# Performance work log

Measured on AMD Instinct MI355X. Metric: run time of the kernel, lower is better.

## Reference

```python
import jax, jax.numpy as jnp
import numpy as np

EMBED = 2048
HEADS = 16
HEAD_DIM = EMBED // HEADS
BATCH = 4
SEQ = 2048


def setup_inputs() -> dict:
    key = jax.random.key(0)
    ks = jax.random.split(key, 9)
    s = 1.0 / np.sqrt(EMBED)
    return {
        "x": jax.random.normal(ks[0], (BATCH, SEQ, EMBED), jnp.float32),
        "q_w": jax.random.normal(ks[1], (EMBED, EMBED), jnp.float32) * s,
        "q_b": jax.random.normal(ks[2], (EMBED,), jnp.float32) * 0.01,
        "k_w": jax.random.normal(ks[3], (EMBED, EMBED), jnp.float32) * s,
        "k_b": jax.random.normal(ks[4], (EMBED,), jnp.float32) * 0.01,
        "v_w": jax.random.normal(ks[5], (EMBED, EMBED), jnp.float32) * s,
        "v_b": jax.random.normal(ks[6], (EMBED,), jnp.float32) * 0.01,
        "o_w": jax.random.normal(ks[7], (EMBED, EMBED), jnp.float32) * s,
        "o_b": jax.random.normal(ks[8], (EMBED,), jnp.float32) * 0.01,
    }


def _split_heads(t):
    B, S, _ = t.shape
    return t.reshape(B, S, HEADS, HEAD_DIM).transpose(0, 2, 1, 3)  # [B,H,S,D]


def reference(x, q_w, q_b, k_w, k_b, v_w, v_b, o_w, o_b):
    B, S, E = x.shape
    q = _split_heads(x @ q_w.T + q_b)
    k = _split_heads(x @ k_w.T + k_b)
    v = _split_heads(x @ v_w.T + v_b)
    scores = jnp.einsum("bhsd,bhtd->bhst", q, k) / np.sqrt(HEAD_DIM).astype(np.float32)
    # ALiBi bias: slopes_i = -2^(-(8-i)); bias = -|s-t| * slope  (faithful to source)
    slopes = jnp.asarray([-2.0 ** (-(8 - i)) for i in range(HEADS)], jnp.float32)
    pos = jnp.arange(S)
    rel = -jnp.abs(pos[None, :] - pos[:, None]).astype(jnp.float32)  # [S,S]
    scores = scores + rel[None, None] * slopes[None, :, None, None]
    attn = jax.nn.softmax(scores, axis=-1)
    out = jnp.einsum("bhst,bhtd->bhsd", attn, v)
    out = out.transpose(0, 2, 1, 3).reshape(B, S, E)
    return out @ o_w.T + o_b
```

## Files before the change

### kernel.cpp

```cpp
#include <hip/hip_runtime.h>

#define EMBED 2048
#define HEADS 16
#define HDIM  128
#define BATCH 4
#define SEQ   2048
#define MROWS (BATCH*SEQ)

typedef __attribute__((ext_vector_type(8))) _Float16 h8;
typedef __attribute__((ext_vector_type(4))) _Float16 h4;
typedef __attribute__((ext_vector_type(4))) float     f32x4;

__device__ inline f32x4 mfma16(h8 a, h8 b, f32x4 c){
  return __builtin_amdgcn_mfma_f32_16x16x32_f16(a, b, c, 0, 0, 0);
}

__device__ inline void gl_lds16(const void* g, void* l){
  __builtin_amdgcn_global_load_lds(
      (__attribute__((address_space(1))) unsigned*)g,
      (__attribute__((address_space(3))) unsigned*)l, 16, 0, 0);
}

__global__ __launch_bounds__(256) void f2h_kernel(const float* __restrict__ src,
                                                  _Float16* __restrict__ dst, int n){
  int stride = gridDim.x * blockDim.x * 8;
  for (int i = (blockIdx.x*blockDim.x + threadIdx.x)*8; i < n; i += stride){
    f32x4 a = *(const f32x4*)(src + i);
    f32x4 b = *(const f32x4*)(src + i + 4);
    h8 o;
    o[0]=(_Float16)a[0]; o[1]=(_Float16)a[1]; o[2]=(_Float16)a[2]; o[3]=(_Float16)a[3];
    o[4]=(_Float16)b[0]; o[5]=(_Float16)b[1]; o[6]=(_Float16)b[2]; o[7]=(_Float16)b[3];
    *(h8*)(dst + i) = o;
  }
}

template<int MODE>
__global__ __launch_bounds__(256) void gemm_bt(const _Float16* __restrict__ A,
                                               const _Float16* __restrict__ Bw,
                                               const float* __restrict__ bias,
                                               void* __restrict__ Cout, int K)
{
  constexpr int BM=128, BN=128, BK=64;
  __shared__ _Float16 Al[BM*BK];
  __shared__ _Float16 Bl[BN*BK];
  const int tid = threadIdx.x;
  const int l = tid & 63, w = tid >> 6;
  const int bm = blockIdx.x * BM, bn = blockIdx.y * BN;
  const int wm = (w & 1) * 64, wn = (w >> 1) * 64;
  const f32x4 zero = {0.f,0.f,0.f,0.f};
  f32x4 acc[4][4];
  #pragma unroll
  for (int mi=0;mi<4;++mi)
    #pragma unroll
    for (int ni=0;ni<4;++ni) acc[mi][ni]=zero;

  for (int kt = 0; kt < K; kt += BK){
    __syncthreads();
    #pragma unroll
    for (int i=0;i<4;++i){
      int row = w*32 + i*8 + (l>>3);
      int col = (l&7)*8;
      gl_lds16(A  + (size_t)(bm+row)*K + kt + col, &Al[(w*32 + i*8)*BK]);
      gl_lds16(Bw + (size_t)(bn+row)*K + kt + col, &Bl[(w*32 + i*8)*BK]);
    }
    __syncthreads();
    #pragma unroll
    for (int ks=0; ks<BK; ks+=32){
      h8 af[4], bf[4];
      #pragma unroll
      for (int mi=0;mi<4;++mi) af[mi] = *(const h8*)&Al[(wm + mi*16 + (l&15))*BK + ks + ((l>>4)*8)];
      #pragma unroll
      for (int ni=0;ni<4;++ni) bf[ni] = *(const h8*)&Bl[(wn + ni*16 + (l&15))*BK + ks + ((l>>4)*8)];
      #pragma unroll
      for (int mi=0;mi<4;++mi)
        #pragma unroll
        for (int ni=0;ni<4;++ni)
          acc[mi][ni] = mfma16(af[mi], bf[ni], acc[mi][ni]);
    }
  }

  #pragma unroll
  for (int ni=0;ni<4;++ni){
    int n = bn + wn + ni*16 + (l & 15);
    float bv = bias[n];
    #pragma unroll
    for (int mi=0;mi<4;++mi){
      int m0 = bm + wm + mi*16 + ((l>>4)*4);
      if constexpr (MODE==0){
        #pragma unroll
        for (int r=0;r<4;++r)
          ((_Float16*)Cout)[(size_t)(m0+r)*EMBED + n] = (_Float16)(acc[mi][ni][r] + bv);
      } else if constexpr (MODE==1){
        #pragma unroll
        for (int r=0;r<4;++r)
          ((float*)Cout)[(size_t)(m0+r)*EMBED + n] = acc[mi][ni][r] + bv;
      } else {
        int b = m0 >> 11, s0 = m0 & (SEQ-1);
        int hh = n >> 7,  d  = n & (HDIM-1);
        h4 pk;
        #pragma unroll
        for (int r=0;r<4;++r) pk[r] = (_Float16)(acc[mi][ni][r] + bv);
        *(h4*)((_Float16*)Cout + ((size_t)(b*HEADS + hh)*HDIM + d)*SEQ + s0) = pk;
      }
    }
  }
}

__global__ __launch_bounds__(256) void attn_kernel(const _Float16* __restrict__ Q,
                                                   const _Float16* __restrict__ Kt,
                                                   const _Float16* __restrict__ Vt_g,
                                                   _Float16* __restrict__ O)
{
  constexpr int QB=64, KB=64;
  __shared__ _Float16 Kl[KB][HDIM+8];
  __shared__ _Float16 Vl[HDIM][KB+8];
  __shared__ _Float16 Pl[4][16][KB+8];
  const int tid = threadIdx.x, l = tid & 63, w = tid >> 6;
  const int bh = blockIdx.y;
  const int b = bh >> 4, h = bh & 15;
  const int q0 = blockIdx.x * QB;
  const float slope = exp2f((float)h - 8.0f);
  const float scale = 0.08838834764831845f;
  const f32x4 zero = {0.f,0.f,0.f,0.f};

  h8 qf[4];
  {
    int qrow = q0 + w*16 + (l & 15);
    const _Float16* qp = Q + (size_t)(b*SEQ + qrow)*EMBED + h*HDIM + ((l>>4)*8);
    #pragma unroll
    for (int ks=0;ks<4;++ks) qf[ks] = *(const h8*)(qp + ks*32);
  }
  float mrow[4], lsum[4];
  f32x4 acc[8];
  #pragma unroll
  for (int df=0;df<8;++df) acc[df]=zero;
  #pragma unroll
  for (int r=0;r<4;++r){ mrow[r] = -3.0e38f; lsum[r] = 0.f; }

  const int sr = tid >> 2;
  const int sd = (tid & 3) * 32;
  const int vdr = tid >> 1;
  const int vss = (tid & 1) * 32;

  for (int kt = 0; kt < SEQ; kt += KB){
    __syncthreads();
    {
      const _Float16* gk = Kt + (size_t)(b*SEQ + kt + sr)*EMBED + h*HDIM + sd;
      h8 k0 = ((const h8*)gk)[0], k1 = ((const h8*)gk)[1],
         k2 = ((const h8*)gk)[2], k3 = ((const h8*)gk)[3];
      *(h8*)&Kl[sr][sd]    = k0;  *(h8*)&Kl[sr][sd+8]  = k1;
      *(h8*)&Kl[sr][sd+16] = k2;  *(h8*)&Kl[sr][sd+24] = k3;
      const _Float16* gv = Vt_g + ((size_t)bh*HDIM + vdr)*SEQ + kt + vss;
      h8 v0 = ((const h8*)gv)[0], v1 = ((const h8*)gv)[1],
         v2 = ((const h8*)gv)[2], v3 = ((const h8*)gv)[3];
      *(h8*)&Vl[vdr][vss]    = v0;  *(h8*)&Vl[vdr][vss+8]  = v1;
      *(h8*)&Vl[vdr][vss+16] = v2;  *(h8*)&Vl[vdr][vss+24] = v3;
    }
    __syncthreads();

    float p[4][4];
    #pragma unroll
    for (int nf=0;nf<4;++nf){
      f32x4 s = zero;
      #pragma unroll
      for (int ks=0;ks<4;++ks){
        h8 kf = *(const h8*)&Kl[nf*16 + (l&15)][ks*32 + ((l>>4)*8)];
        s = mfma16(qf[ks], kf, s);
      }
      int tcol = kt + nf*16 + (l & 15);
      #pragma unroll
      for (int r=0;r<4;++r){
        int qr = q0 + w*16 + ((l>>4)*4) + r;
        p[nf][r] = s[r]*scale + slope*fabsf((float)(qr - tcol));
      }
    }
    float pm[4];
    #pragma unroll
    for (int r=0;r<4;++r)
      pm[r] = fmaxf(fmaxf(p[0][r],p[1][r]), fmaxf(p[2][r],p[3][r]));
    #pragma unroll
    for (int off=1; off<16; off<<=1){
      #pragma unroll
      for (int r=0;r<4;++r) pm[r] = fmaxf(pm[r], __shfl_xor(pm[r], off));
    }
    float rs[4];
    #pragma unroll
    for (int r=0;r<4;++r){
      float mn = fmaxf(mrow[r], pm[r]);
      float sc = __expf(mrow[r] - mn);
      mrow[r] = mn;
      lsum[r] *= sc;
      rs[r] = 0.f;
      #pragma unroll
      for (int nf=0;nf<4;++nf){
        p[nf][r] = __expf(p[nf][r] - mn);
        rs[r] += p[nf][r];
      }
      #pragma unroll
      for (int df=0;df<8;++df) acc[df][r] *= sc;
    }
    #pragma unroll
    for (int off=1; off<16; off<<=1){
      #pragma unroll
      for (int r=0;r<4;++r) rs[r] += __shfl_xor(rs[r], off);
    }
    #pragma unroll
    for (int r=0;r<4;++r) lsum[r] += rs[r];

    #pragma unroll
    for (int nf=0;nf<4;++nf)
      #pragma unroll
      for (int r=0;r<4;++r)
        Pl[w][((l>>4)*4)+r][nf*16 + (l&15)] = (_Float16)p[nf][r];
    #pragma unroll
    for (int ks=0; ks<2; ++ks){
      h8 pf = *(const h8*)&Pl[w][l & 15][ks*32 + ((l>>4)*8)];
      #pragma unroll
      for (int df=0; df<8; ++df){
        h8 vf = *(const h8*)&Vl[df*16 + (l&15)][ks*32 + ((l>>4)*8)];
        acc[df] = mfma16(pf, vf, acc[df]);
      }
    }
  }
  #pragma unroll
  for (int df=0; df<8; ++df){
    int d = df*16 + (l & 15);
    #pragma unroll
    for (int r=0;r<4;++r){
      int s = q0 + w*16 + ((l>>4)*4) + r;
      float v = acc[df][r] / lsum[r];
      O[(size_t)(b*SEQ + s)*EMBED + h*HDIM + d] = (_Float16)v;
    }
  }
}

extern "C" void kernel_launch(void* const* d_in, const int* in_sizes, int n_in,
                              void* d_out, int out_size, void* d_ws, size_t ws_size,
                              hipStream_t stream)
{
  const float* x   = (const float*)d_in[0];
  const float* q_w = (const float*)d_in[1];
  const float* q_b = (const float*)d_in[2];
  const float* k_w = (const float*)d_in[3];
  const float* k_b = (const float*)d_in[4];
  const float* v_w = (const float*)d_in[5];
  const float* v_b = (const float*)d_in[6];
  const float* o_w = (const float*)d_in[7];
  const float* o_b = (const float*)d_in[8];

  char* ws = (char*)d_ws;
  _Float16* xh = (_Float16*)(ws);
  _Float16* wq = (_Float16*)(ws + 33554432);
  _Float16* wk = (_Float16*)(ws + 41943040);
  _Float16* wv = (_Float16*)(ws + 50331648);
  _Float16* wo = (_Float16*)(ws + 58720256);
  _Float16* Qf = (_Float16*)(ws + 67108864);
  _Float16* Kf = (_Float16*)(ws + 100663296);
  _Float16* Vt = (_Float16*)(ws + 134217728);
  _Float16* Ah = xh;

  f2h_kernel<<<1024, 256, 0, stream>>>(x,   xh, MROWS*EMBED);
  f2h_kernel<<<512,  256, 0, stream>>>(q_w, wq, EMBED*EMBED);
  f2h_kernel<<<512,  256, 0, stream>>>(k_w, wk, EMBED*EMBED);
  f2h_kernel<<<512,  256, 0, stream>>>(v_w, wv, EMBED*EMBED);
  f2h_kernel<<<512,  256, 0, stream>>>(o_w, wo, EMBED*EMBED);

  dim3 gg(MROWS/128, EMBED/128);
  gemm_bt<0><<<gg, 256, 0, stream>>>(xh, wq, q_b, (void*)Qf, EMBED);
  gemm_bt<0><<<gg, 256, 0, stream>>>(xh, wk, k_b, (void*)Kf, EMBED);
  gemm_bt<2><<<gg, 256, 0, stream>>>(xh, wv, v_b, (void*)Vt, EMBED);

  dim3 ga(SEQ/64, BATCH*HEADS);
  attn_kernel<<<ga, 256, 0, stream>>>(Qf, Kf, Vt, Ah);

  gemm_bt<1><<<gg, 256, 0, stream>>>(Ah, wo, o_b, d_out, EMBED);
}
```

Baseline: 942.6 us.

## Rewrite attention with 32x32 MFMA, swizzled LDS, register P, lazy rescale

The attention kernel is restructured to use 32x32x16 MFMA with S computed transposed (K as A operand), so P can be rebuilt in registers via pkrtz and cross-half shuffles instead of a round trip through LDS. K/V tiles use XOR-swizzled LDS layouts without padding, blocks grow to 512 threads covering 256 queries each with an XCD-aware block remap, and softmax uses exp2 with prescaled constants plus a threshold-based lazy rescale of the accumulator. This aims to cut LDS traffic and softmax overhead and to share each K/V tile across more queries. In exchange it adds register pressure, and the lazy rescale can let intermediate values grow by up to 2^11 before renormalising.

```diff
diff --git a/kernel.cpp b/kernel.cpp
--- a/kernel.cpp
+++ b/kernel.cpp
@@ -7,14 +7,22 @@
 #define SEQ   2048
 #define MROWS (BATCH*SEQ)
 
-typedef __attribute__((ext_vector_type(8))) _Float16 h8;
-typedef __attribute__((ext_vector_type(4))) _Float16 h4;
-typedef __attribute__((ext_vector_type(4))) float     f32x4;
+typedef __attribute__((ext_vector_type(8)))  _Float16 h8;
+typedef __attribute__((ext_vector_type(4)))  _Float16 h4;
+typedef __attribute__((ext_vector_type(4)))  float    f32x4;
+typedef __attribute__((ext_vector_type(16))) float    f32x16;
+typedef __attribute__((ext_vector_type(4)))  unsigned u32x4;
 
 __device__ inline f32x4 mfma16(h8 a, h8 b, f32x4 c){
   return __builtin_amdgcn_mfma_f32_16x16x32_f16(a, b, c, 0, 0, 0);
 }
-
+__device__ inline f32x16 mfma32(h8 a, h8 b, f32x16 c){
+  return __builtin_amdgcn_mfma_f32_32x32x16_f16(a, b, c, 0, 0, 0);
+}
+__device__ inline unsigned pkrtz(float a, float b){
+  auto t = __builtin_amdgcn_cvt_pkrtz(a, b);
+  return __builtin_bit_cast(unsigned, t);
+}
 __device__ inline void gl_lds16(const void* g, void* l){
   __builtin_amdgcn_global_load_lds(
       (__attribute__((address_space(1))) unsigned*)g,
@@ -41,8 +49,8 @@
                                                void* __restrict__ Cout, int K)
 {
   constexpr int BM=128, BN=128, BK=64;
-  __shared__ _Float16 Al[BM*BK];
-  __shared__ _Float16 Bl[BN*BK];
+  __shared__ __align__(16) _Float16 Al[BM*BK];
+  __shared__ __align__(16) _Float16 Bl[BN*BK];
   const int tid = threadIdx.x;
   const int l = tid & 63, w = tid >> 6;
   const int bm = blockIdx.x * BM, bn = blockIdx.y * BN;
@@ -106,131 +114,153 @@
   }
 }
 
-__global__ __launch_bounds__(256) void attn_kernel(const _Float16* __restrict__ Q,
-                                                   const _Float16* __restrict__ Kt,
-                                                   const _Float16* __restrict__ Vt_g,
-                                                   _Float16* __restrict__ O)
+__global__ __launch_bounds__(512, 2) void attn_kernel(const _Float16* __restrict__ Qf,
+                                                      const _Float16* __restrict__ Kf,
+                                                      const _Float16* __restrict__ Vt,
+                                                      _Float16* __restrict__ O)
 {
-  constexpr int QB=64, KB=64;
-  __shared__ _Float16 Kl[KB][HDIM+8];
-  __shared__ _Float16 Vl[HDIM][KB+8];
-  __shared__ _Float16 Pl[4][16][KB+8];
-  const int tid = threadIdx.x, l = tid & 63, w = tid >> 6;
-  const int bh = blockIdx.y;
+  __shared__ __align__(16) _Float16 Kl[64*128];
+  __shared__ __align__(16) _Float16 Vl[128*64];
+  char* klb = (char*)Kl; char* vlb = (char*)Vl;
+
+  const int tid = threadIdx.x;
+  const int l = tid & 63, w = tid >> 6;
+  const int l31 = l & 31, hi = l >> 5;
+  const int bid = blockIdx.x;
+  const int swz = (bid & 7)*64 + (bid >> 3);
+  const int bh = swz >> 3, qt = swz & 7;
   const int b = bh >> 4, h = bh & 15;
-  const int q0 = blockIdx.x * QB;
-  const float slope = exp2f((float)h - 8.0f);
-  const float scale = 0.08838834764831845f;
-  const f32x4 zero = {0.f,0.f,0.f,0.f};
-
-  h8 qf[4];
+  const int q0w = qt*256 + w*32;
+
+  const float slope2 = exp2f((float)(h - 8)) * 1.44269504f;
+  const float scale2 = 0.08838834764831845f * 1.44269504f;
+
+  h8 qfr[8];
   {
-    int qrow = q0 + w*16 + (l & 15);
-    const _Float16* qp = Q + (size_t)(b*SEQ + qrow)*EMBED + h*HDIM + ((l>>4)*8);
-    #pragma unroll
-    for (int ks=0;ks<4;++ks) qf[ks] = *(const h8*)(qp + ks*32);
-  }
-  float mrow[4], lsum[4];
-  f32x4 acc[8];
+    const _Float16* qp = Qf + ((size_t)(b*SEQ) + q0w + l31)*EMBED + h*HDIM + hi*8;
+    #pragma unroll
+    for (int ks=0;ks<8;++ks) qfr[ks] = *(const h8*)(qp + ks*16);
+  }
+
+  f32x16 acc[4];
   #pragma unroll
-  for (int df=0;df<8;++df) acc[df]=zero;
-  #pragma unroll
-  for (int r=0;r<4;++r){ mrow[r] = -3.0e38f; lsum[r] = 0.f; }
-
-  const int sr = tid >> 2;
-  const int sd = (tid & 3) * 32;
-  const int vdr = tid >> 1;
-  const int vss = (tid & 1) * 32;
-
-  for (int kt = 0; kt < SEQ; kt += KB){
+  for (int d=0; d<4; ++d)
+    #pragma unroll
+    for (int i=0; i<16; ++i) acc[d][i] = 0.f;
+  float m = -1e9f, lsum = 0.f;
+
+  const int krow = tid >> 3, kcol = tid & 7;
+  const int vrow = tid >> 2, vcol = tid & 3;
+  const _Float16* kg = Kf + ((size_t)(b*SEQ) + krow)*EMBED + h*HDIM + kcol*16;
+  const _Float16* vg = Vt + ((size_t)bh*HDIM + vrow)*SEQ + vcol*16;
+  const unsigned kb0 = (unsigned)(krow*256 + kcol*32)      ^ ((krow&7)<<4);
+  const unsigned kb1 = (unsigned)(krow*256 + kcol*32 + 16) ^ ((krow&7)<<4);
+  const unsigned vb0 = (unsigned)(vrow*128 + vcol*32)      ^ ((vrow&7)<<4);
+  const unsigned vb1 = (unsigned)(vrow*128 + vcol*32 + 16) ^ ((vrow&7)<<4);
+
+  const float qv = (float)(q0w + l31);
+  const int sw7 = (l & 7) << 4;
+
+  for (int kt = 0; kt < SEQ; kt += 64){
     __syncthreads();
     {
-      const _Float16* gk = Kt + (size_t)(b*SEQ + kt + sr)*EMBED + h*HDIM + sd;
-      h8 k0 = ((const h8*)gk)[0], k1 = ((const h8*)gk)[1],
-         k2 = ((const h8*)gk)[2], k3 = ((const h8*)gk)[3];
-      *(h8*)&Kl[sr][sd]    = k0;  *(h8*)&Kl[sr][sd+8]  = k1;
-      *(h8*)&Kl[sr][sd+16] = k2;  *(h8*)&Kl[sr][sd+24] = k3;
-      const _Float16* gv = Vt_g + ((size_t)bh*HDIM + vdr)*SEQ + kt + vss;
-      h8 v0 = ((const h8*)gv)[0], v1 = ((const h8*)gv)[1],
-         v2 = ((const h8*)gv)[2], v3 = ((const h8*)gv)[3];
-      *(h8*)&Vl[vdr][vss]    = v0;  *(h8*)&Vl[vdr][vss+8]  = v1;
-      *(h8*)&Vl[vdr][vss+16] = v2;  *(h8*)&Vl[vdr][vss+24] = v3;
+      h8 a0 = *(const h8*)(kg); h8 a1 = *(const h8*)(kg + 8);
+      h8 c0 = *(const h8*)(vg); h8 c1 = *(const h8*)(vg + 8);
+      *(h8*)(klb + kb0) = a0; *(h8*)(klb + kb1) = a1;
+      *(h8*)(vlb + vb0) = c0; *(h8*)(vlb + vb1) = c1;
+      kg += (size_t)64*EMBED; vg += 64;
     }
     __syncthreads();
 
-    float p[4][4];
-    #pragma unroll
-    for (int nf=0;nf<4;++nf){
-      f32x4 s = zero;
-      #pragma unroll
-      for (int ks=0;ks<4;++ks){
-        h8 kf = *(const h8*)&Kl[nf*16 + (l&15)][ks*32 + ((l>>4)*8)];
-        s = mfma16(qf[ks], kf, s);
+    f32x16 s0, s1;
+    #pragma unroll
+    for (int i=0;i<16;++i){ s0[i]=0.f; s1[i]=0.f; }
+    #pragma unroll
+    for (int ks=0;ks<8;++ks){
+      int colb = ks*32 + hi*16;
+      h8 k0 = *(const h8*)(klb + (((l31     )*256 + colb) ^ sw7));
+      h8 k1 = *(const h8*)(klb + (((l31 + 32)*256 + colb) ^ sw7));
+      s0 = mfma32(k0, qfr[ks], s0);
+      s1 = mfma32(k1, qfr[ks], s1);
+    }
+
+    float a0r[16], a1r[16];
+    float pm = -1e9f;
+    const float tb = (float)kt;
+    #pragma unroll
+    for (int i=0;i<16;++i){
+      float pat = (float)((i&3) + 8*(i>>2) + hi*4);
+      float t0 = tb + pat, t1 = tb + 32.f + pat;
+      a0r[i] = fmaf(slope2, fabsf(qv - t0), s0[i]*scale2);
+      a1r[i] = fmaf(slope2, fabsf(qv - t1), s1[i]*scale2);
+      pm = fmaxf(pm, fmaxf(a0r[i], a1r[i]));
+    }
+    pm = fmaxf(pm, __shfl_xor(pm, 32));
+
+    if (__any(pm > m + 11.f)){
+      float mn = fmaxf(m, pm);
+      float sc = exp2f(m - mn);
+      m = mn; lsum *= sc;
+      #pragma unroll
+      for (int i=0;i<16;++i){
+        float scv = __shfl(sc, (i&3) + 8*(i>>2) + hi*4);
+        #pragma unroll
+        for (int d=0;d<4;++d) acc[d][i] *= scv;
       }
-      int tcol = kt + nf*16 + (l & 15);
-      #pragma unroll
-      for (int r=0;r<4;++r){
-        int qr = q0 + w*16 + ((l>>4)*4) + r;
-        p[nf][r] = s[r]*scale + slope*fabsf((float)(qr - tcol));
+    }
+
+    float p0[16], p1[16];
+    float rs = 0.f;
+    #pragma unroll
+    for (int i=0;i<16;++i){
+      p0[i] = exp2f(a0r[i] - m);
+      p1[i] = exp2f(a1r[i] - m);
+      rs += p0[i] + p1[i];
+    }
+    lsum += rs + __shfl_xor(rs, 32);
+
+    unsigned paw[4][4];
+    {
+      auto buildP = [&](const float (&p)[16], int tt){
+        #pragma unroll
+        for (int hf=0; hf<2; ++hf){
+          const int E = hf*8;
+          unsigned A0 = pkrtz(p[E+0], p[E+1]), A1 = pkrtz(p[E+2], p[E+3]);
+          unsigned B0 = pkrtz(p[E+4], p[E+5]), B1 = pkrtz(p[E+6], p[E+7]);
+          unsigned sA0 = __shfl_xor(A0, 32), sA1 = __shfl_xor(A1, 32);
+          unsigned sB0 = __shfl_xor(B0, 32), sB1 = __shfl_xor(B1, 32);
+          const int ks = tt*2 + hf;
+          paw[ks][0] = hi ? sB0 : A0;
+          paw[ks][1] = hi ? sB1 : A1;
+          paw[ks][2] = hi ? B0  : sA0;
+          paw[ks][3] = hi ? B1  : sA1;
+        }
+      };
+      buildP(p0, 0);
+      buildP(p1, 1);
+    }
+
+    #pragma unroll
+    for (int ks=0; ks<4; ++ks){
+      u32x4 pw = {paw[ks][0], paw[ks][1], paw[ks][2], paw[ks][3]};
+      h8 pa = __builtin_bit_cast(h8, pw);
+      #pragma unroll
+      for (int d=0; d<4; ++d){
+        h8 vf = *(const h8*)(vlb + (((d*32 + l31)*128 + ks*32 + hi*16) ^ sw7));
+        acc[d] = mfma32(pa, vf, acc[d]);
       }
     }
-    float pm[4];
-    #pragma unroll
-    for (int r=0;r<4;++r)
-      pm[r] = fmaxf(fmaxf(p[0][r],p[1][r]), fmaxf(p[2][r],p[3][r]));
-    #pragma unroll
-    for (int off=1; off<16; off<<=1){
-      #pragma unroll
-      for (int r=0;r<4;++r) pm[r] = fmaxf(pm[r], __shfl_xor(pm[r], off));
-    }
-    float rs[4];
-    #pragma unroll
-    for (int r=0;r<4;++r){
-      float mn = fmaxf(mrow[r], pm[r]);
-      float sc = __expf(mrow[r] - mn);
-      mrow[r] = mn;
-      lsum[r] *= sc;
-      rs[r] = 0.f;
-      #pragma unroll
-      for (int nf=0;nf<4;++nf){
-        p[nf][r] = __expf(p[nf][r] - mn);
-        rs[r] += p[nf][r];
-      }
-      #pragma unroll
-      for (int df=0;df<8;++df) acc[df][r] *= sc;
-    }
-    #pragma unroll
-    for (int off=1; off<16; off<<=1){
-      #pragma unroll
-      for (int r=0;r<4;++r) rs[r] += __shfl_xor(rs[r], off);
-    }
-    #pragma unroll
-    for (int r=0;r<4;++r) lsum[r] += rs[r];
-
-    #pragma unroll
-    for (int nf=0;nf<4;++nf)
-      #pragma unroll
-      for (int r=0;r<4;++r)
-        Pl[w][((l>>4)*4)+r][nf*16 + (l&15)] = (_Float16)p[nf][r];
-    #pragma unroll
-    for (int ks=0; ks<2; ++ks){
-      h8 pf = *(const h8*)&Pl[w][l & 15][ks*32 + ((l>>4)*8)];
-      #pragma unroll
-      for (int df=0; df<8; ++df){
-        h8 vf = *(const h8*)&Vl[df*16 + (l&15)][ks*32 + ((l>>4)*8)];
-        acc[df] = mfma16(pf, vf, acc[df]);
-      }
-    }
-  }
+  }
+
+  float inv = 1.0f / lsum;
+  _Float16* ob = O + ((size_t)(b*SEQ) + q0w)*EMBED + h*HDIM + l31;
   #pragma unroll
-  for (int df=0; df<8; ++df){
-    int d = df*16 + (l & 15);
-    #pragma unroll
-    for (int r=0;r<4;++r){
-      int s = q0 + w*16 + ((l>>4)*4) + r;
-      float v = acc[df][r] / lsum[r];
-      O[(size_t)(b*SEQ + s)*EMBED + h*HDIM + d] = (_Float16)v;
-    }
+  for (int i=0;i<16;++i){
+    int ql = (i&3) + 8*(i>>2) + hi*4;
+    float iq = __shfl(inv, ql);
+    #pragma unroll
+    for (int d=0;d<4;++d)
+      ob[(size_t)ql*EMBED + d*32] = (_Float16)(acc[d][i] * iq);
   }
 }
 
@@ -270,8 +300,7 @@
   gemm_bt<0><<<gg, 256, 0, stream>>>(xh, wk, k_b, (void*)Kf, EMBED);
   gemm_bt<2><<<gg, 256, 0, stream>>>(xh, wv, v_b, (void*)Vt, EMBED);
 
-  dim3 ga(SEQ/64, BATCH*HEADS);
-  attn_kernel<<<ga, 256, 0, stream>>>(Qf, Kf, Vt, Ah);
+  attn_kernel<<<512, 512, 0, stream>>>(Qf, Kf, Vt, Ah);
 
   gemm_bt<1><<<gg, 256, 0, stream>>>(Ah, wo, o_b, d_out, EMBED);
 }
```

New measurement: 781.3 us. -17.1%, faster.
